# Kernel tuning notes

Hardware: AMD Instinct MI355X
Metric: run time of the kernel (lower is better)

The kernel has to match this reference:

```python
import jax, jax.numpy as jnp
import numpy as np

W_EDGE, W_LAP, W_NORMAL, W_VEL = 0.5, 0.05, 0.01, 10.0


def _grid_mesh(g):
    ids = np.arange(g * g).reshape(g, g)
    tl, tr = ids[:-1, :-1].ravel(), ids[:-1, 1:].ravel()
    bl, br = ids[1:, :-1].ravel(), ids[1:, 1:].ravel()
    f1 = np.stack([tl, bl, br], 1)
    f2 = np.stack([tl, br, tr], 1)
    return np.concatenate([f1, f2], 0).astype(np.int64)  # [F,3]


def _topology(faces):
    # all directed edges with the opposite vertex of their face
    e = np.concatenate([faces[:, [0, 1]], faces[:, [1, 2]], faces[:, [2, 0]]], 0)
    opp = np.concatenate([faces[:, 2], faces[:, 0], faces[:, 1]], 0)
    key = np.sort(e, axis=1)
    uniq, inv = np.unique(key, axis=0, return_inverse=True)  # unique undirected edges
    counts = np.bincount(inv)
    order = np.argsort(inv, kind='stable')
    sel = counts[inv[order]] == 2
    idx2 = order[sel].reshape(-1, 2)  # the two face-slots of each interior edge
    ekey = key[idx2[:, 0]]
    pairs = np.stack([ekey[:, 0], ekey[:, 1], opp[idx2[:, 0]], opp[idx2[:, 1]]], 1)
    return uniq.astype(np.int64), pairs.astype(np.int64)


def setup_inputs() -> dict:
    key = jax.random.key(0)
    k1, k2 = jax.random.split(key)
    B, g = 2, 91
    N = g * g  # 8281
    faces = _grid_mesh(g)                 # [16200,3]
    edges, nc_pairs = _topology(faces)    # [24480,2], [24120,4]
    predictions = jax.random.normal(k1, (B, N, 3), dtype=jnp.float32)
    targets = jax.random.normal(k2, (B, N, 3), dtype=jnp.float32)
    return {
        'predictions': predictions,
        'targets': targets,
        'pred_faces': jnp.asarray(faces),
        'edges': jnp.asarray(edges),
        'nc_pairs': jnp.asarray(nc_pairs),
    }


def _chamfer(x, y):
    # pytorch3d chamfer_distance: squared dists, point mean both ways, batch mean
    xx = jnp.sum(x * x, -1)
    yy = jnp.sum(y * y, -1)
    d = xx[:, :, None] + yy[:, None, :] - 2.0 * jnp.einsum('bnd,bmd->bnm', x, y)
    d = jnp.maximum(d, 0.0)
    return jnp.mean(jnp.min(d, axis=2).mean(axis=1) + jnp.min(d, axis=1).mean(axis=1))


def _edge_loss(verts, edges):
    # mean over meshes of mean over edges of squared edge length (target len 0)
    ve = verts[:, edges]  # [B,E,2,3]
    l2 = jnp.sum((ve[:, :, 0] - ve[:, :, 1]) ** 2, -1)
    return l2.mean()


def _cot_laplacian_loss_one(verts, faces):
    # verts [N,3]; pytorch3d cot_laplacian + method='cot' smoothing
    fv = verts[faces]  # [F,3,3]
    v0, v1, v2 = fv[:, 0], fv[:, 1], fv[:, 2]
    A = jnp.linalg.norm(v1 - v2, axis=1)
    Bl = jnp.linalg.norm(v0 - v2, axis=1)
    C = jnp.linalg.norm(v0 - v1, axis=1)
    s = 0.5 * (A + Bl + C)
    area = jnp.sqrt(jnp.maximum(s * (s - A) * (s - Bl) * (s - C), 1e-12))
    A2, B2, C2 = A * A, Bl * Bl, C * C
    cota = (B2 + C2 - A2) / area
    cotb = (A2 + C2 - B2) / area
    cotc = (A2 + B2 - C2) / area
    cot = jnp.stack([cota, cotb, cotc], 1) / 4.0  # [F,3]
    ii = faces[:, jnp.array([1, 2, 0])]
    jj = faces[:, jnp.array([2, 0, 1])]
    i = jnp.concatenate([ii, jj], 0).ravel()
    j = jnp.concatenate([jj, ii], 0).ravel()
    w = jnp.concatenate([cot, cot], 0).ravel()
    N = verts.shape[0]
    Lx = jnp.zeros_like(verts).at[i].add(w[:, None] * verts[j])
    rowsum = jnp.zeros((N,), dtype=verts.dtype).at[i].add(w)
    norm_w = jnp.where(rowsum > 0, 1.0 / rowsum, 0.0)
    res = Lx * norm_w[:, None] - verts
    return jnp.linalg.norm(res, axis=1).mean()


def _normal_consistency_one(verts, pairs):
    # pairs [P,4] = (v0, v1, opp_a, opp_b) per interior edge
    p = verts[pairs]  # [P,4,3]
    e = p[:, 1] - p[:, 0]
    n0 = jnp.cross(e, p[:, 2] - p[:, 0])
    n1 = -jnp.cross(e, p[:, 3] - p[:, 0])
    eps = 1e-8
    cos = jnp.sum(n0 * n1, -1) / (
        jnp.maximum(jnp.linalg.norm(n0, axis=1), eps)
        * jnp.maximum(jnp.linalg.norm(n1, axis=1), eps)
    )
    return (1.0 - cos).mean()


def _forward(predictions, targets, pred_faces, edges, nc_pairs):
    loss_cham = _chamfer(predictions, targets)
    edge_l = _edge_loss(predictions, edges)
    lap_l = jax.vmap(lambda v: _cot_laplacian_loss_one(v, pred_faces))(predictions).mean()
    nc_l = jax.vmap(lambda v: _normal_consistency_one(v, nc_pairs))(predictions).mean()
    pred_shift = predictions[:, 1:, :] - predictions[:, :-1, :]
    tgt_shift = targets[:, 1:, :] - targets[:, :-1, :]
    vel_l = _chamfer(pred_shift, tgt_shift)
    return loss_cham + W_LAP * lap_l + W_NORMAL * nc_l + W_EDGE * edge_l + W_VEL * vel_l


def reference(predictions, targets, pred_faces, edges, nc_pairs):
    return _forward(predictions, targets, pred_faces, edges, nc_pairs)
```

## Files before the change

kernel.cpp:

```cpp
#include <hip/hip_runtime.h>


#define W_EDGE   0.5f
#define W_LAP    0.05f
#define W_NORMAL 0.01f
#define W_VEL    10.0f

#define NX  7
#define TPB 128
#define YT  256

__device__ __forceinline__ float wave_sum(float v) {
#pragma unroll
    for (int o = 32; o > 0; o >>= 1) v += __shfl_down(v, o, 64);
    return v;
}

__global__ void init_ws_k(float* __restrict__ ws, int nzero, int ninf)
{
    unsigned int* w = (unsigned int*)ws;
    const int total = nzero + ninf;
    for (int i = blockIdx.x * blockDim.x + threadIdx.x; i < total;
         i += gridDim.x * blockDim.x)
        w[i] = (i < nzero) ? 0u : 0x7F7F7F7Fu;
}

__global__ __launch_bounds__(TPB)
void chamfer_all_k(const float* __restrict__ pred, const float* __restrict__ tgt,
                   int N, unsigned int* __restrict__ mins)
{
    const int variant = blockIdx.z >> 1;
    const int b       = blockIdx.z & 1;
    const int shift   = variant >> 1;
    const int Np      = N - shift;
    const int N1      = N - 1;

    const float* __restrict__ xb = ((variant & 1) == 0 ? pred : tgt) + (size_t)b * N * 3;
    const float* __restrict__ yb = ((variant & 1) == 0 ? tgt : pred) + (size_t)b * N * 3;

    size_t off;
    if (variant == 0)      off = (size_t)b * N;
    else if (variant == 1) off = (size_t)2 * N + (size_t)b * N;
    else if (variant == 2) off = (size_t)4 * N + (size_t)b * N1;
    else                   off = (size_t)4 * N + (size_t)2 * N1 + (size_t)b * N1;
    unsigned int* __restrict__ out = mins + off;

    const int base = blockIdx.x * (TPB * NX) + threadIdx.x;

    float xs0[NX], xs1[NX], xs2[NX], xx[NX], m[NX];
#pragma unroll
    for (int k = 0; k < NX; ++k) {
        const int gi = base + k * TPB;
        float a0 = 0.f, a1 = 0.f, a2 = 0.f;
        if (gi < Np) {
            if (shift) {
                a0 = xb[(gi + 1) * 3 + 0] - xb[gi * 3 + 0];
                a1 = xb[(gi + 1) * 3 + 1] - xb[gi * 3 + 1];
                a2 = xb[(gi + 1) * 3 + 2] - xb[gi * 3 + 2];
            } else {
                a0 = xb[gi * 3 + 0]; a1 = xb[gi * 3 + 1]; a2 = xb[gi * 3 + 2];
            }
        }
        xx[k]  = fmaf(a0, a0, fmaf(a1, a1, a2 * a2));
        xs0[k] = -2.0f * a0; xs1[k] = -2.0f * a1; xs2[k] = -2.0f * a2;
        m[k]   = 3.0e38f;
    }

    __shared__ float4 sy[YT];
    const int ys = blockIdx.y * YT;
#pragma unroll
    for (int r = 0; r < YT / TPB; ++r) {
        const int j  = threadIdx.x + r * TPB;
        const int yi = ys + j;
        float4 v = make_float4(0.f, 0.f, 0.f, 3.0e38f);
        if (yi < Np) {
            float y0, y1, y2;
            if (shift) {
                y0 = yb[(yi + 1) * 3 + 0] - yb[yi * 3 + 0];
                y1 = yb[(yi + 1) * 3 + 1] - yb[yi * 3 + 1];
                y2 = yb[(yi + 1) * 3 + 2] - yb[yi * 3 + 2];
            } else {
                y0 = yb[yi * 3 + 0]; y1 = yb[yi * 3 + 1]; y2 = yb[yi * 3 + 2];
            }
            v = make_float4(y0, y1, y2, fmaf(y0, y0, fmaf(y1, y1, y2 * y2)));
        }
        sy[j] = v;
    }
    __syncthreads();

#pragma unroll 8
    for (int jj = 0; jj < YT; ++jj) {
        const float4 y = sy[jj];
#pragma unroll
        for (int k = 0; k < NX; ++k) {
            float u = fmaf(xs0[k], y.x, fmaf(xs1[k], y.y, fmaf(xs2[k], y.z, y.w)));
            m[k] = fminf(m[k], u);
        }
    }

#pragma unroll
    for (int k = 0; k < NX; ++k) {
        const int gi = base + k * TPB;
        if (gi < Np) {
            const float d = fmaxf(xx[k] + m[k], 0.0f);
            atomicMin(&out[gi], __float_as_uint(d));
        }
    }
}

__global__ void mesh_k(const float* __restrict__ pred,
                       const int* __restrict__ edges, int E,
                       const int* __restrict__ pairs, int P,
                       const int* __restrict__ faces, int F,
                       int N, int B, float scaleE, float scaleP,
                       float* __restrict__ Lx, float* __restrict__ rowsum,
                       float* __restrict__ accum)
{
    const int tE = B * E, tP = B * P, tF = B * F;
    const int total = tE + tP + tF;
    float se = 0.f, sp = 0.f;
    for (int idx = blockIdx.x * blockDim.x + threadIdx.x; idx < total;
         idx += gridDim.x * blockDim.x) {
        if (idx < tE) {
            const int b = idx / E;
            const int e = idx - b * E;
            const float* __restrict__ vb = pred + (size_t)b * N * 3;
            const int i0 = edges[e * 2 + 0], i1 = edges[e * 2 + 1];
            float dx = vb[i0 * 3 + 0] - vb[i1 * 3 + 0];
            float dy = vb[i0 * 3 + 1] - vb[i1 * 3 + 1];
            float dz = vb[i0 * 3 + 2] - vb[i1 * 3 + 2];
            se += fmaf(dx, dx, fmaf(dy, dy, dz * dz));
        } else if (idx < tE + tP) {
            const int q = idx - tE;
            const int b = q / P;
            const int p = q - b * P;
            const float* __restrict__ vb = pred + (size_t)b * N * 3;
            const int a0 = pairs[p * 4 + 0], a1 = pairs[p * 4 + 1];
            const int a2 = pairs[p * 4 + 2], a3 = pairs[p * 4 + 3];
            float p0x = vb[a0 * 3], p0y = vb[a0 * 3 + 1], p0z = vb[a0 * 3 + 2];
            float ex = vb[a1 * 3] - p0x, ey = vb[a1 * 3 + 1] - p0y, ez = vb[a1 * 3 + 2] - p0z;
            float ux = vb[a2 * 3] - p0x, uy = vb[a2 * 3 + 1] - p0y, uz = vb[a2 * 3 + 2] - p0z;
            float wx = vb[a3 * 3] - p0x, wy = vb[a3 * 3 + 1] - p0y, wz = vb[a3 * 3 + 2] - p0z;
            float n0x = ey * uz - ez * uy;
            float n0y = ez * ux - ex * uz;
            float n0z = ex * uy - ey * ux;
            float n1x = -(ey * wz - ez * wy);
            float n1y = -(ez * wx - ex * wz);
            float n1z = -(ex * wy - ey * wx);
            float dt = n0x * n1x + n0y * n1y + n0z * n1z;
            float l0 = sqrtf(n0x * n0x + n0y * n0y + n0z * n0z);
            float l1 = sqrtf(n1x * n1x + n1y * n1y + n1z * n1z);
            sp += 1.0f - dt / (fmaxf(l0, 1e-8f) * fmaxf(l1, 1e-8f));
        } else {
            const int q = idx - tE - tP;
            const int b = q / F;
            const int f = q - b * F;
            const float* __restrict__ vb = pred + (size_t)b * N * 3;
            const int i0 = faces[f * 3 + 0], i1 = faces[f * 3 + 1], i2 = faces[f * 3 + 2];
            float v0x = vb[i0 * 3], v0y = vb[i0 * 3 + 1], v0z = vb[i0 * 3 + 2];
            float v1x = vb[i1 * 3], v1y = vb[i1 * 3 + 1], v1z = vb[i1 * 3 + 2];
            float v2x = vb[i2 * 3], v2y = vb[i2 * 3 + 1], v2z = vb[i2 * 3 + 2];
            float ax = v1x - v2x, ay = v1y - v2y, az = v1z - v2z;
            float bx = v0x - v2x, by = v0y - v2y, bz = v0z - v2z;
            float cx = v0x - v1x, cy = v0y - v1y, cz = v0z - v1z;
            float A  = sqrtf(ax * ax + ay * ay + az * az);
            float Bl = sqrtf(bx * bx + by * by + bz * bz);
            float C  = sqrtf(cx * cx + cy * cy + cz * cz);
            float s2 = 0.5f * (A + Bl + C);
            float area = sqrtf(fmaxf(s2 * (s2 - A) * (s2 - Bl) * (s2 - C), 1e-12f));
            float A2 = A * A, B2 = Bl * Bl, C2 = C * C;
            float inv4a = 1.0f / (4.0f * area);
            float cota = (B2 + C2 - A2) * inv4a;
            float cotb = (A2 + C2 - B2) * inv4a;
            float cotc = (A2 + B2 - C2) * inv4a;

            float* __restrict__ Lb = Lx + (size_t)b * N * 3;
            float* __restrict__ rb = rowsum + (size_t)b * N;
            #define SCAT(i, j, w)                                             \
                atomicAdd(&Lb[(i) * 3 + 0], (w) * vb[(j) * 3 + 0]);           \
                atomicAdd(&Lb[(i) * 3 + 1], (w) * vb[(j) * 3 + 1]);           \
                atomicAdd(&Lb[(i) * 3 + 2], (w) * vb[(j) * 3 + 2]);           \
                atomicAdd(&rb[(i)], (w));
            SCAT(i1, i2, cota) SCAT(i2, i1, cota)
            SCAT(i2, i0, cotb) SCAT(i0, i2, cotb)
            SCAT(i0, i1, cotc) SCAT(i1, i0, cotc)
            #undef SCAT
        }
    }
    se = wave_sum(se);
    sp = wave_sum(sp);
    if ((threadIdx.x & 63) == 0) atomicAdd(accum, fmaf(se, scaleE, sp * scaleP));
}

__global__ void finalize_k(const unsigned int* __restrict__ mins, int lenN2, int lenN12,
                           float sA, float sC,
                           const float* __restrict__ pred, const float* __restrict__ Lx,
                           const float* __restrict__ rowsum, int N, int B, float scaleL,
                           float* __restrict__ accum)
{
    const int tM = lenN2 + lenN12;
    const int total = tM + B * N;
    float s1 = 0.f, s2 = 0.f, s3 = 0.f;
    for (int idx = blockIdx.x * blockDim.x + threadIdx.x; idx < total;
         idx += gridDim.x * blockDim.x) {
        if (idx < lenN2)      s1 += __uint_as_float(mins[idx]);
        else if (idx < tM)    s2 += __uint_as_float(mins[idx]);
        else {
            const int q = idx - tM;
            float rs = rowsum[q];
            float nw = rs > 0.f ? 1.0f / rs : 0.f;
            float rx = Lx[q * 3 + 0] * nw - pred[q * 3 + 0];
            float ry = Lx[q * 3 + 1] * nw - pred[q * 3 + 1];
            float rz = Lx[q * 3 + 2] * nw - pred[q * 3 + 2];
            s3 += sqrtf(rx * rx + ry * ry + rz * rz);
        }
    }
    s1 = wave_sum(s1);
    s2 = wave_sum(s2);
    s3 = wave_sum(s3);
    if ((threadIdx.x & 63) == 0)
        atomicAdd(accum, fmaf(s1, sA, fmaf(s2, sC, s3 * scaleL)));
}

__global__ void write_out_k(const float* __restrict__ accum, float* __restrict__ out)
{
    out[0] = accum[0];
}

extern "C" void kernel_launch(void* const* d_in, const int* in_sizes, int n_in,
                              void* d_out, int out_size, void* d_ws, size_t ws_size,
                              hipStream_t stream)
{
    const float* pred = (const float*)d_in[0];
    const float* tgt  = (const float*)d_in[1];
    const int* faces  = (const int*)d_in[2];
    const int* edges  = (const int*)d_in[3];
    const int* pairs  = (const int*)d_in[4];

    const int B = 2;
    const int N = in_sizes[0] / (3 * B);
    const int F = in_sizes[2] / 3;
    const int E = in_sizes[3] / 2;
    const int P = in_sizes[4] / 4;
    const int N1 = N - 1;

    float* ws       = (float*)d_ws;
    float* accum    = ws;
    float* Lx       = ws + 8;
    float* rowsum   = Lx + (size_t)B * N * 3;
    unsigned int* minsBase = (unsigned int*)(rowsum + (size_t)B * N);

    const int nzero = 8 + B * N * 3 + B * N;
    const int ninf  = 2 * B * N + 2 * B * N1;

    init_ws_k<<<64, dim3(256), 0, stream>>>(ws, nzero, ninf);

    const dim3 gc((N + TPB * NX - 1) / (TPB * NX), (N + YT - 1) / YT, 4 * B);
    chamfer_all_k<<<gc, dim3(TPB), 0, stream>>>(pred, tgt, N, minsBase);

    mesh_k<<<128, dim3(256), 0, stream>>>(pred, edges, E, pairs, P, faces, F, N, B,
                                          W_EDGE / ((float)B * (float)E),
                                          W_NORMAL / ((float)B * (float)P),
                                          Lx, rowsum, accum);

    const float sBN  = 1.0f / ((float)B * (float)N);
    const float sBN1 = W_VEL / ((float)B * (float)N1);
    finalize_k<<<96, dim3(256), 0, stream>>>(minsBase, 2 * B * N, 2 * B * N1, sBN, sBN1,
                                             pred, Lx, rowsum, N, B,
                                             W_LAP / ((float)B * (float)N), accum);

    write_out_k<<<1, 1, 0, stream>>>(accum, (float*)d_out);
}
```

Measured before the change: 82.40 us.

## Compute chamfer distances with bf16 split-precision MFMA and shared row/column minima

Replaces the scalar FMA chamfer kernel with one that builds the squared-distance matrix using 32x32x16 bf16 MFMA instructions. Operands are split into hi/lo bf16 parts to approximate fp32 accuracy, and norm terms are folded into the matrix product. One pass now yields both row minima (kept in registers) and column minima (shared-memory atomics with ordered keys), so the symmetric x->y and y->x passes are no longer computed separately. Target fragments are precomputed by a new prep kernel. The split-bf16 scheme risks precision loss relative to fp32.

After: 102.3 us. 24.2% more time.

```diff
diff --git a/kernel.cpp b/kernel.cpp
--- a/kernel.cpp
+++ b/kernel.cpp
@@ -1,14 +1,33 @@
 #include <hip/hip_runtime.h>
 
+
+typedef unsigned int uint32;
+typedef __attribute__((ext_vector_type(8)))  short bf16x8;
+typedef __attribute__((ext_vector_type(16))) float f32x16;
 
 #define W_EDGE   0.5f
 #define W_LAP    0.05f
 #define W_NORMAL 0.01f
 #define W_VEL    10.0f
-
-#define NX  7
-#define TPB 128
-#define YT  256
+#define BIGF     3.0e38f
+#define RSTRIDE  8320
+
+__device__ __forceinline__ unsigned short f2bf(float f){
+    uint32 b = __float_as_uint(f);
+    b += 0x7FFFu + ((b >> 16) & 1u);
+    return (unsigned short)(b >> 16);
+}
+__device__ __forceinline__ float bf2f(unsigned short h){
+    return __uint_as_float(((uint32)h) << 16);
+}
+__device__ __forceinline__ uint32 fkey(float f){
+    uint32 b = __float_as_uint(f);
+    return b ^ ((uint32)((int)b >> 31) | 0x80000000u);
+}
+__device__ __forceinline__ float funkey(uint32 k){
+    uint32 b = (k & 0x80000000u) ? (k ^ 0x80000000u) : ~k;
+    return __uint_as_float(b);
+}
 
 __device__ __forceinline__ float wave_sum(float v) {
 #pragma unroll
@@ -18,93 +37,168 @@
 
 __global__ void init_ws_k(float* __restrict__ ws, int nzero, int ninf)
 {
-    unsigned int* w = (unsigned int*)ws;
+    uint32* w = (uint32*)ws;
     const int total = nzero + ninf;
     for (int i = blockIdx.x * blockDim.x + threadIdx.x; i < total;
          i += gridDim.x * blockDim.x)
-        w[i] = (i < nzero) ? 0u : 0x7F7F7F7Fu;
-}
-
-__global__ __launch_bounds__(TPB)
-void chamfer_all_k(const float* __restrict__ pred, const float* __restrict__ tgt,
-                   int N, unsigned int* __restrict__ mins)
-{
-    const int variant = blockIdx.z >> 1;
-    const int b       = blockIdx.z & 1;
-    const int shift   = variant >> 1;
-    const int Np      = N - shift;
-    const int N1      = N - 1;
-
-    const float* __restrict__ xb = ((variant & 1) == 0 ? pred : tgt) + (size_t)b * N * 3;
-    const float* __restrict__ yb = ((variant & 1) == 0 ? tgt : pred) + (size_t)b * N * 3;
-
-    size_t off;
-    if (variant == 0)      off = (size_t)b * N;
-    else if (variant == 1) off = (size_t)2 * N + (size_t)b * N;
-    else if (variant == 2) off = (size_t)4 * N + (size_t)b * N1;
-    else                   off = (size_t)4 * N + (size_t)2 * N1 + (size_t)b * N1;
-    unsigned int* __restrict__ out = mins + off;
-
-    const int base = blockIdx.x * (TPB * NX) + threadIdx.x;
-
-    float xs0[NX], xs1[NX], xs2[NX], xx[NX], m[NX];
-#pragma unroll
-    for (int k = 0; k < NX; ++k) {
-        const int gi = base + k * TPB;
-        float a0 = 0.f, a1 = 0.f, a2 = 0.f;
-        if (gi < Np) {
-            if (shift) {
-                a0 = xb[(gi + 1) * 3 + 0] - xb[gi * 3 + 0];
-                a1 = xb[(gi + 1) * 3 + 1] - xb[gi * 3 + 1];
-                a2 = xb[(gi + 1) * 3 + 2] - xb[gi * 3 + 2];
-            } else {
-                a0 = xb[gi * 3 + 0]; a1 = xb[gi * 3 + 1]; a2 = xb[gi * 3 + 2];
-            }
-        }
-        xx[k]  = fmaf(a0, a0, fmaf(a1, a1, a2 * a2));
-        xs0[k] = -2.0f * a0; xs1[k] = -2.0f * a1; xs2[k] = -2.0f * a2;
-        m[k]   = 3.0e38f;
-    }
-
-    __shared__ float4 sy[YT];
-    const int ys = blockIdx.y * YT;
-#pragma unroll
-    for (int r = 0; r < YT / TPB; ++r) {
-        const int j  = threadIdx.x + r * TPB;
-        const int yi = ys + j;
-        float4 v = make_float4(0.f, 0.f, 0.f, 3.0e38f);
-        if (yi < Np) {
-            float y0, y1, y2;
-            if (shift) {
-                y0 = yb[(yi + 1) * 3 + 0] - yb[yi * 3 + 0];
-                y1 = yb[(yi + 1) * 3 + 1] - yb[yi * 3 + 1];
-                y2 = yb[(yi + 1) * 3 + 2] - yb[yi * 3 + 2];
-            } else {
-                y0 = yb[yi * 3 + 0]; y1 = yb[yi * 3 + 1]; y2 = yb[yi * 3 + 2];
-            }
-            v = make_float4(y0, y1, y2, fmaf(y0, y0, fmaf(y1, y1, y2 * y2)));
-        }
-        sy[j] = v;
-    }
+        w[i] = (i < nzero) ? 0u : 0xFFFFFFFFu;
+}
+
+__global__ void bprep_k(const float* __restrict__ tgt, int N, uint4* __restrict__ bfrag)
+{
+    const int NT = (N + 31) >> 5;
+    const int gt = blockIdx.x * 4 + (threadIdx.x >> 6);
+    if (gt >= 4 * NT) return;
+    const int c = gt / NT, t = gt - c * NT;
+    const int ds = c >> 1, b = c & 1;
+    const int Np = N - ds;
+    const int l = threadIdx.x & 63;
+    const int col = t * 32 + (l & 31);
+    const float* __restrict__ yb = tgt + (size_t)b * N * 3;
+    float y0 = 0.f, y1 = 0.f, y2 = 0.f;
+    const bool valid = col < Np;
+    if (valid){
+        if (ds){
+            y0 = yb[(col+1)*3+0] - yb[col*3+0];
+            y1 = yb[(col+1)*3+1] - yb[col*3+1];
+            y2 = yb[(col+1)*3+2] - yb[col*3+2];
+        } else {
+            y0 = yb[col*3+0]; y1 = yb[col*3+1]; y2 = yb[col*3+2];
+        }
+    }
+    const float yy = fmaf(y0,y0, fmaf(y1,y1, y2*y2));
+    unsigned short yh0=f2bf(y0), yh1=f2bf(y1), yh2=f2bf(y2);
+    unsigned short yl0=f2bf(y0-bf2f(yh0)), yl1=f2bf(y1-bf2f(yh1)), yl2=f2bf(y2-bf2f(yh2));
+    unsigned short yyh, yyl;
+    if (valid){ yyh = f2bf(yy); yyl = f2bf(yy - bf2f(yyh)); }
+    else      { yyh = f2bf(BIGF); yyl = 0; }
+    const short ONE = (short)0x3F80;
+    bf16x8 Bu, Bv;
+    if (l < 32){
+        Bu[0]=(short)yh0; Bu[1]=(short)yh1; Bu[2]=(short)yh2;
+        Bu[3]=(short)yh0; Bu[4]=(short)yh1; Bu[5]=(short)yh2;
+        Bu[6]=(short)yl0; Bu[7]=(short)yl1;
+        Bv = Bu;
+    } else {
+        Bu[0]=(short)yl2; Bu[1]=0;   Bu[2]=0;   Bu[3]=(short)yyh; Bu[4]=(short)yyl;
+        Bu[5]=0; Bu[6]=0; Bu[7]=0;
+        Bv[0]=(short)yl2; Bv[1]=ONE; Bv[2]=ONE; Bv[3]=0;          Bv[4]=0;
+        Bv[5]=0; Bv[6]=0; Bv[7]=0;
+    }
+    const size_t base = (size_t)(c * NT + t) * 128 + l;
+    bfrag[base]      = __builtin_bit_cast(uint4, Bu);
+    bfrag[base + 64] = __builtin_bit_cast(uint4, Bv);
+}
+
+__global__ __launch_bounds__(256)
+void chamfer_mfma_k(const float* __restrict__ pred, int N,
+                    const uint4* __restrict__ bfrag,
+                    float* __restrict__ rowpart, uint32* __restrict__ colmin)
+{
+    const int c = blockIdx.z, ds = c >> 1, b = c & 1;
+    const int Np = N - ds;
+    const int NT = (N + 31) >> 5;
+    const int TC = (NT + 3) >> 2;
+    const int t0 = blockIdx.y * TC;
+    const int t1 = min(NT, t0 + TC);
+    const int w = threadIdx.x >> 6, l = threadIdx.x & 63;
+    const int h = l >> 5;
+    const int grow = blockIdx.x * 128 + w * 32 + (l & 31);
+
+    const float* __restrict__ xb = pred + (size_t)b * N * 3;
+    float a0 = 0.f, a1 = 0.f, a2 = 0.f;
+    const bool xvalid = grow < Np;
+    if (xvalid){
+        if (ds){
+            a0 = xb[(grow+1)*3+0] - xb[grow*3+0];
+            a1 = xb[(grow+1)*3+1] - xb[grow*3+1];
+            a2 = xb[(grow+1)*3+2] - xb[grow*3+2];
+        } else {
+            a0 = xb[grow*3+0]; a1 = xb[grow*3+1]; a2 = xb[grow*3+2];
+        }
+    }
+    const float xx = fmaf(a0,a0, fmaf(a1,a1, a2*a2));
+    unsigned short xh0=f2bf(a0), xh1=f2bf(a1), xh2=f2bf(a2);
+    unsigned short nxh0=f2bf(-2.f*bf2f(xh0)), nxh1=f2bf(-2.f*bf2f(xh1)), nxh2=f2bf(-2.f*bf2f(xh2));
+    unsigned short nxl0=f2bf(-2.f*(a0-bf2f(xh0))), nxl1=f2bf(-2.f*(a1-bf2f(xh1))),
+                   nxl2=f2bf(-2.f*(a2-bf2f(xh2)));
+    const float xxf = xvalid ? xx : BIGF;
+    unsigned short xxh=f2bf(xxf), xxl=f2bf(xxf-bf2f(xxh));
+    const short ONE = (short)0x3F80;
+    bf16x8 A;
+    if (h == 0){
+        A[0]=(short)nxh0; A[1]=(short)nxh1; A[2]=(short)nxh2;
+        A[3]=(short)nxl0; A[4]=(short)nxl1; A[5]=(short)nxl2;
+        A[6]=(short)nxh0; A[7]=(short)nxh1;
+    } else {
+        A[0]=(short)nxh2; A[1]=(short)xxh; A[2]=(short)xxl;
+        A[3]=ONE; A[4]=ONE; A[5]=0; A[6]=0; A[7]=0;
+    }
+
+    const float xxst = xvalid ? xx : 0.f;
+    float xxr[16];
+#pragma unroll
+    for (int r = 0; r < 16; ++r)
+        xxr[r] = __shfl(xxst, (r&3) + 8*(r>>2) + 4*h, 64);
+
+    __shared__ uint32 cl[2080];
+    for (int i = threadIdx.x; i < TC*32; i += 256) cl[i] = 0xFFFFFFFFu;
     __syncthreads();
 
-#pragma unroll 8
-    for (int jj = 0; jj < YT; ++jj) {
-        const float4 y = sy[jj];
-#pragma unroll
-        for (int k = 0; k < NX; ++k) {
-            float u = fmaf(xs0[k], y.x, fmaf(xs1[k], y.y, fmaf(xs2[k], y.z, y.w)));
-            m[k] = fminf(m[k], u);
-        }
-    }
-
-#pragma unroll
-    for (int k = 0; k < NX; ++k) {
-        const int gi = base + k * TPB;
-        if (gi < Np) {
-            const float d = fmaxf(xx[k] + m[k], 0.0f);
-            atomicMin(&out[gi], __float_as_uint(d));
-        }
+    float rm[16];
+#pragma unroll
+    for (int r = 0; r < 16; ++r) rm[r] = BIGF;
+    f32x16 zacc;
+#pragma unroll
+    for (int r = 0; r < 16; ++r) zacc[r] = 0.f;
+
+    const uint4* __restrict__ bfp = bfrag + (size_t)c * NT * 128 + l;
+
+    for (int t = t0; t < t1; ++t){
+        const bf16x8 Bu = __builtin_bit_cast(bf16x8, bfp[(size_t)t*128]);
+        const bf16x8 Bv = __builtin_bit_cast(bf16x8, bfp[(size_t)t*128 + 64]);
+        const f32x16 au = __builtin_amdgcn_mfma_f32_32x32x16_bf16(A, Bu, zacc, 0, 0, 0);
+        const f32x16 av = __builtin_amdgcn_mfma_f32_32x32x16_bf16(A, Bv, zacc, 0, 0, 0);
+#pragma unroll
+        for (int r = 0; r < 16; ++r) rm[r] = fminf(rm[r], au[r]);
+        float cv = fminf(fminf(av[0],  av[1]),  av[2]);
+        cv = fminf(fminf(cv, av[3]),  av[4]);
+        cv = fminf(fminf(cv, av[5]),  av[6]);
+        cv = fminf(fminf(cv, av[7]),  av[8]);
+        cv = fminf(fminf(cv, av[9]),  av[10]);
+        cv = fminf(fminf(cv, av[11]), av[12]);
+        cv = fminf(fminf(cv, av[13]), av[14]);
+        cv = fminf(cv, av[15]);
+        cv = fminf(cv, __shfl_xor(cv, 32, 64));
+        if (l < 32) atomicMin(&cl[(t - t0)*32 + l], fkey(cv));
+    }
+
+#pragma unroll
+    for (int r = 0; r < 16; ++r){
+        float v = rm[r];
+        v = fminf(v, __shfl_xor(v, 1, 64));
+        v = fminf(v, __shfl_xor(v, 2, 64));
+        v = fminf(v, __shfl_xor(v, 4, 64));
+        v = fminf(v, __shfl_xor(v, 8, 64));
+        v = fminf(v, __shfl_xor(v, 16, 64));
+        rm[r] = v;
+    }
+    float* __restrict__ rp = rowpart + (size_t)(c*4 + blockIdx.y) * RSTRIDE;
+#pragma unroll
+    for (int r = 0; r < 16; ++r){
+        if ((l & 31) == r){
+            const int rowl = (r&3) + 8*(r>>2) + 4*h;
+            const int gr = blockIdx.x * 128 + w * 32 + rowl;
+            if (gr < Np) rp[gr] = rm[r] + xxr[r];
+        }
+    }
+
+    __syncthreads();
+    const int ncols = (t1 - t0) * 32;
+    uint32* __restrict__ cm = colmin + (size_t)c * RSTRIDE;
+    for (int i = threadIdx.x; i < ncols; i += 256){
+        const int col = t0*32 + i;
+        if (col < Np) atomicMin(&cm[col], cl[i]);
     }
 }
 
@@ -176,11 +270,11 @@
 
             float* __restrict__ Lb = Lx + (size_t)b * N * 3;
             float* __restrict__ rb = rowsum + (size_t)b * N;
-            #define SCAT(i, j, w)                                             \
-                atomicAdd(&Lb[(i) * 3 + 0], (w) * vb[(j) * 3 + 0]);           \
-                atomicAdd(&Lb[(i) * 3 + 1], (w) * vb[(j) * 3 + 1]);           \
-                atomicAdd(&Lb[(i) * 3 + 2], (w) * vb[(j) * 3 + 2]);           \
-                atomicAdd(&rb[(i)], (w));
+            #define SCAT(i, j, wv)                                            \
+                atomicAdd(&Lb[(i) * 3 + 0], (wv) * vb[(j) * 3 + 0]);          \
+                atomicAdd(&Lb[(i) * 3 + 1], (wv) * vb[(j) * 3 + 1]);          \
+                atomicAdd(&Lb[(i) * 3 + 2], (wv) * vb[(j) * 3 + 2]);          \
+                atomicAdd(&rb[(i)], (wv));
             SCAT(i1, i2, cota) SCAT(i2, i1, cota)
             SCAT(i2, i0, cotb) SCAT(i0, i2, cotb)
             SCAT(i0, i1, cotc) SCAT(i1, i0, cotc)
@@ -192,34 +286,56 @@
     if ((threadIdx.x & 63) == 0) atomicAdd(accum, fmaf(se, scaleE, sp * scaleP));
 }
 
-__global__ void finalize_k(const unsigned int* __restrict__ mins, int lenN2, int lenN12,
-                           float sA, float sC,
-                           const float* __restrict__ pred, const float* __restrict__ Lx,
-                           const float* __restrict__ rowsum, int N, int B, float scaleL,
+__global__ void finalize_k(const float* __restrict__ rowpart, const uint32* __restrict__ colmin,
+                           const float* __restrict__ tgt, const float* __restrict__ pred,
+                           const float* __restrict__ Lx, const float* __restrict__ rowsum,
+                           int N, float sMain, float sVel, float scaleL,
                            float* __restrict__ accum)
 {
-    const int tM = lenN2 + lenN12;
-    const int total = tM + B * N;
-    float s1 = 0.f, s2 = 0.f, s3 = 0.f;
+    const int total = 8 * N + 2 * N;
+    float sm = 0.f, sv = 0.f, sl = 0.f;
     for (int idx = blockIdx.x * blockDim.x + threadIdx.x; idx < total;
          idx += gridDim.x * blockDim.x) {
-        if (idx < lenN2)      s1 += __uint_as_float(mins[idx]);
-        else if (idx < tM)    s2 += __uint_as_float(mins[idx]);
-        else {
-            const int q = idx - tM;
+        if (idx < 4 * N) {
+            const int c = idx / N, i = idx - c * N;
+            const int ds = c >> 1;
+            if (i < N - ds) {
+                const float* rp = rowpart + (size_t)c * 4 * RSTRIDE;
+                float v = fminf(fminf(rp[i], rp[RSTRIDE + i]),
+                                fminf(rp[2*RSTRIDE + i], rp[3*RSTRIDE + i]));
+                float d = fmaxf(v, 0.f);
+                if (ds) sv += d; else sm += d;
+            }
+        } else if (idx < 8 * N) {
+            const int q = idx - 4 * N;
+            const int c = q / N, j = q - c * N;
+            const int ds = c >> 1, b = c & 1;
+            if (j < N - ds) {
+                const float* __restrict__ yb = tgt + (size_t)b * N * 3;
+                float y0, y1, y2;
+                if (ds) {
+                    y0 = yb[(j+1)*3+0] - yb[j*3+0];
+                    y1 = yb[(j+1)*3+1] - yb[j*3+1];
+                    y2 = yb[(j+1)*3+2] - yb[j*3+2];
+                } else { y0 = yb[j*3+0]; y1 = yb[j*3+1]; y2 = yb[j*3+2]; }
+                float yy = fmaf(y0,y0, fmaf(y1,y1, y2*y2));
+                float v = funkey(colmin[(size_t)c * RSTRIDE + j]) + yy;
+                float d = fmaxf(v, 0.f);
+                if (ds) sv += d; else sm += d;
+            }
+        } else {
+            const int q = idx - 8 * N;
             float rs = rowsum[q];
             float nw = rs > 0.f ? 1.0f / rs : 0.f;
-            float rx = Lx[q * 3 + 0] * nw - pred[q * 3 + 0];
-            float ry = Lx[q * 3 + 1] * nw - pred[q * 3 + 1];
-            float rz = Lx[q * 3 + 2] * nw - pred[q * 3 + 2];
-            s3 += sqrtf(rx * rx + ry * ry + rz * rz);
-        }
-    }
-    s1 = wave_sum(s1);
-    s2 = wave_sum(s2);
-    s3 = wave_sum(s3);
+            float rx = Lx[q*3+0]*nw - pred[q*3+0];
+            float ry = Lx[q*3+1]*nw - pred[q*3+1];
+            float rz = Lx[q*3+2]*nw - pred[q*3+2];
+            sl += sqrtf(rx*rx + ry*ry + rz*rz);
+        }
+    }
+    sm = wave_sum(sm); sv = wave_sum(sv); sl = wave_sum(sl);
     if ((threadIdx.x & 63) == 0)
-        atomicAdd(accum, fmaf(s1, sA, fmaf(s2, sC, s3 * scaleL)));
+        atomicAdd(accum, fmaf(sm, sMain, fmaf(sv, sVel, sl * scaleL)));
 }
 
 __global__ void write_out_k(const float* __restrict__ accum, float* __restrict__ out)
@@ -242,31 +358,35 @@
     const int F = in_sizes[2] / 3;
     const int E = in_sizes[3] / 2;
     const int P = in_sizes[4] / 4;
-    const int N1 = N - 1;
-
-    float* ws       = (float*)d_ws;
-    float* accum    = ws;
-    float* Lx       = ws + 8;
-    float* rowsum   = Lx + (size_t)B * N * 3;
-    unsigned int* minsBase = (unsigned int*)(rowsum + (size_t)B * N);
+    const int NT = (N + 31) >> 5;
+
+    float* ws      = (float*)d_ws;
+    float* accum   = ws;
+    float* Lx      = ws + 8;
+    float* rowsum  = Lx + (size_t)B * N * 3;
+    uint32* colmin = (uint32*)(rowsum + (size_t)B * N);
+    float* rowpart = (float*)(colmin + 4 * RSTRIDE);
+    size_t off     = 8 + (size_t)B*N*3 + (size_t)B*N + 4*RSTRIDE + 16*RSTRIDE;
+    uint4* bfrag   = (uint4*)(ws + off);
 
     const int nzero = 8 + B * N * 3 + B * N;
-    const int ninf  = 2 * B * N + 2 * B * N1;
+    const int ninf  = 4 * RSTRIDE;
 
     init_ws_k<<<64, dim3(256), 0, stream>>>(ws, nzero, ninf);
 
-    const dim3 gc((N + TPB * NX - 1) / (TPB * NX), (N + YT - 1) / YT, 4 * B);
-    chamfer_all_k<<<gc, dim3(TPB), 0, stream>>>(pred, tgt, N, minsBase);
+    bprep_k<<<dim3(NT), dim3(256), 0, stream>>>(tgt, N, bfrag);
+
+    chamfer_mfma_k<<<dim3((N + 127) / 128, 4, 4), dim3(256), 0, stream>>>(
+        pred, N, bfrag, rowpart, colmin);
 
     mesh_k<<<128, dim3(256), 0, stream>>>(pred, edges, E, pairs, P, faces, F, N, B,
                                           W_EDGE / ((float)B * (float)E),
                                           W_NORMAL / ((float)B * (float)P),
                                           Lx, rowsum, accum);
 
-    const float sBN  = 1.0f / ((float)B * (float)N);
-    const float sBN1 = W_VEL / ((float)B * (float)N1);
-    finalize_k<<<96, dim3(256), 0, stream>>>(minsBase, 2 * B * N, 2 * B * N1, sBN, sBN1,
-                                             pred, Lx, rowsum, N, B,
+    finalize_k<<<96, dim3(256), 0, stream>>>(rowpart, colmin, tgt, pred, Lx, rowsum, N,
+                                             1.0f / ((float)B * (float)N),
+                                             W_VEL / ((float)B * (float)(N - 1)),
                                              W_LAP / ((float)B * (float)N), accum);
 
     write_out_k<<<1, 1, 0, stream>>>(accum, (float*)d_out);
```
